# Performance work log

Hardware: AMD Instinct MI355X
Metric: run time of the kernel (lower is better)

Reference implementation:

```python
import jax, jax.numpy as jnp
import numpy as np

N = 8192        # num_nodes
H = 128         # h_dim
E = 131072      # num edges (avg degree 16)
NREL = 90       # num relations
NB = 8          # num_bases (block-diagonal decomposition)
SI = H // NB    # block size 16


def setup_inputs() -> dict:
    key = jax.random.key(0)
    ks = jax.random.split(key, 24)
    sc = 0.01
    n = lambda k, shape, s=sc: jax.random.normal(k, shape, dtype=jnp.float32) * s
    return {
        'node_ids': jnp.arange(N, dtype=jnp.int32),
        'src': jax.random.randint(ks[0], (E,), 0, N, dtype=jnp.int32),
        'dst': jax.random.randint(ks[1], (E,), 0, N, dtype=jnp.int32),
        'etypes': jax.random.randint(ks[2], (E,), 0, NREL, dtype=jnp.int32),
        'norm': jax.random.uniform(ks[3], (E, 1), dtype=jnp.float32),
        'eps': jax.random.normal(ks[4], (N, H), dtype=jnp.float32),
        # input embedding layer
        'embedding': n(ks[5], (N, H)),
        # RelGraphConv layer 0 ('bdd'): per-relation block-diag weights, self-loop, bias
        'W0': n(ks[6], (NREL, NB, SI, SI)),
        'loop0': n(ks[7], (H, H)),
        'b0': jnp.zeros((H,), jnp.float32),
        # RelGraphConv layer 1
        'W1': n(ks[8], (NREL, NB, SI, SI)),
        'loop1': n(ks[9], (H, H)),
        'b1': jnp.zeros((H,), jnp.float32),
        # z_layer: Linear(H, 2H)  (weights stored as (in, out))
        'Wz': n(ks[10], (H, 2 * H)),
        'bz': jnp.zeros((2 * H,), jnp.float32),
        # inter_layer (UpdateLayer): Linear(H, H) + h_bias
        'Wi': n(ks[11], (H, H)),
        'bi': jnp.zeros((H,), jnp.float32),
        'hbi': jnp.zeros((H,), jnp.float32),
        # output_layer (second UpdateLayer)
        'Wo': n(ks[12], (H, H)),
        'bo': jnp.zeros((H,), jnp.float32),
        'hbo': jnp.zeros((H,), jnp.float32),
    }


def _rgcn_bdd(h, W, loop_w, bias, src, dst, etypes, norm, act):
    # gather src features, split into NB blocks of size SI
    x = h[src].reshape(-1, NB, SI)                       # [E, NB, SI]
    Wg = W[etypes]                                       # [E, NB, SI, SI] per-edge relation block weights
    msg = jnp.einsum('ebi,ebio->ebo', x, Wg).reshape(-1, H) * norm  # [E, H]
    agg = jax.ops.segment_sum(msg, dst, num_segments=N)  # scatter-add to dst
    out = agg + bias + h @ loop_w                        # self-loop + bias
    return act(out) if act is not None else out


def reference(node_ids, src, dst, etypes, norm, eps, embedding,
              W0, loop0, b0, W1, loop1, b1,
              Wz, bz, Wi, bi, hbi, Wo, bo, hbo):
    # input layer: embedding lookup; saved as input_embed
    x0 = embedding[node_ids]                             # [N, H]
    h = _rgcn_bdd(x0, W0, loop0, b0, src, dst, etypes, norm, jax.nn.relu)
    h = _rgcn_bdd(h, W1, loop1, b1, src, dst, etypes, norm, None)
    # VAE head: z ~ N(mean, exp(log_std))
    zml = h @ Wz + bz                                    # [N, 2H]
    z_mean, z_log_std = jnp.split(zml, 2, axis=-1)
    z = z_mean + jnp.exp(z_log_std) * eps                # reparameterized sample
    # decode 1: outer-product reconstruction + fused update
    R = z @ z.T                                          # [N, N]
    h = R @ (z @ Wi + bi) + R @ x0 + hbi
    # decode 2
    R2 = h @ h.T                                         # [N, N]
    out = R2 @ (h @ Wo + bo) + R2 @ x0 + hbo
    return out
```

## Files before the change

### kernel.cpp

```cpp
#include <hip/hip_runtime.h>
#include <hip/hip_bf16.h>
#include <math.h>

#define Hdim 128
#define NBq 8
#define SIq 16

typedef __attribute__((ext_vector_type(8))) short short8x;
typedef __attribute__((ext_vector_type(4))) float f32x4;
typedef __attribute__((ext_vector_type(4))) unsigned short ushort4x;
typedef __attribute__((ext_vector_type(2))) _Float16 half2x;

__device__ inline unsigned short f2b(float f) {
  unsigned int u = __float_as_uint(f);
  return (unsigned short)((u + 0x7fffu + ((u >> 16) & 1u)) >> 16);
}
__device__ inline unsigned int pack2(float lo, float hi) {
  return (unsigned int)f2b(lo) | ((unsigned int)f2b(hi) << 16);
}
__device__ inline unsigned short f2h(float f) {
  _Float16 h = (_Float16)f;
  unsigned short u;
  __builtin_memcpy(&u, &h, 2);
  return u;
}
__device__ inline half2x u2h(unsigned int u) {
  union { unsigned int u; half2x h; } v;
  v.u = u;
  return v.h;
}

__global__ __launch_bounds__(256) void k_pre(
    const float* __restrict__ emb, const int* __restrict__ ids, float* __restrict__ x0,
    unsigned short* __restrict__ x0h,
    const float* __restrict__ W0, unsigned short* __restrict__ Wt0,
    const float* __restrict__ W1, unsigned short* __restrict__ Wt1, int w0elems,
    const float* __restrict__ l0, const float* __restrict__ l1,
    const float* __restrict__ Wi, const float* __restrict__ Wo, const float* __restrict__ Wz,
    unsigned short* __restrict__ l0t, unsigned short* __restrict__ l1t,
    unsigned short* __restrict__ Wit, unsigned short* __restrict__ Wot,
    unsigned short* __restrict__ Wzt,
    const int* __restrict__ dst, int* __restrict__ cnt, int E,
    int b1, int b2, int b3) {
  int bx = blockIdx.x, t = threadIdx.x;
  if (bx < b1) {
    int idx = bx * 256 + t;
    int n = idx >> 5, c4 = idx & 31;
    int s = ids[n];
    float4 v = ((const float4*)emb)[(size_t)s * 32 + c4];
    ((float4*)x0)[(size_t)n * 32 + c4] = v;
    ushort4x h;
    h.x = f2h(v.x); h.y = f2h(v.y); h.z = f2h(v.z); h.w = f2h(v.w);
    ((ushort4x*)x0h)[(size_t)n * 32 + c4] = h;
  } else if (bx < b2) {
    int idx = (bx - b1) * 256 + t;
    const float* W = (idx < w0elems) ? W0 : W1;
    unsigned short* Wt = (idx < w0elems) ? Wt0 : Wt1;
    int local = (idx < w0elems) ? idx : idx - w0elems;
    int rb = local >> 8, io = local & 255;
    int i = io >> 4, o = io & 15;
    Wt[(size_t)rb * 256 + o * 16 + i] = f2h(W[(size_t)rb * 256 + i * 16 + o]);
  } else if (bx < b3) {
    int idx = (bx - b2) * 256 + t;
    if (idx < 65536) {
      int w = idx >> 14, local = idx & 16383;
      const float* in = (w == 0) ? l0 : (w == 1) ? l1 : (w == 2) ? Wi : Wo;
      unsigned short* out = (w == 0) ? l0t : (w == 1) ? l1t : (w == 2) ? Wit : Wot;
      int n = local >> 7, k = local & 127;
      out[local] = f2b(in[k * 128 + n]);
    } else {
      int local = idx - 65536;
      int n = local >> 7, k = local & 127;
      Wzt[local] = f2b(Wz[k * 256 + n]);
    }
  } else {
    int e = (bx - b3) * 256 + t;
    if (e < E) atomicAdd(&cnt[dst[e]], 1);
  }
}

__global__ __launch_bounds__(1024) void k_scan(const int* __restrict__ cnt,
                                               int* __restrict__ off,
                                               int* __restrict__ cur, int N, int E) {
  __shared__ int part[1024];
  int t = threadIdx.x;
  int ipt = N / 1024;
  int base = t * ipt;
  int loc[8];
  int s = 0;
  for (int i = 0; i < ipt; ++i) { loc[i] = s; s += cnt[base + i]; }
  part[t] = s;
  __syncthreads();
  for (int d = 1; d < 1024; d <<= 1) {
    int v = part[t];
    int add = (t >= d) ? part[t - d] : 0;
    __syncthreads();
    part[t] = v + add;
    __syncthreads();
  }
  int pre = (t == 0) ? 0 : part[t - 1];
  for (int i = 0; i < ipt; ++i) {
    int o = pre + loc[i];
    off[base + i] = o;
    cur[base + i] = o;
  }
  if (t == 0) off[N] = E;
}

__global__ void k_scatter(const int* __restrict__ src, const int* __restrict__ dst,
                          const int* __restrict__ et, const float* __restrict__ norm,
                          int* __restrict__ cur, int* __restrict__ psrc,
                          int* __restrict__ pet, float* __restrict__ pnorm, int E) {
  int e = blockIdx.x * blockDim.x + threadIdx.x;
  if (e >= E) return;
  int p = atomicAdd(&cur[dst[e]], 1);
  psrc[p] = src[e];
  pet[p]  = et[e];
  pnorm[p] = norm[e];
}

__global__ __launch_bounds__(128) void k_edge(
    const unsigned short* __restrict__ xh, const unsigned short* __restrict__ Wt,
    const int* __restrict__ off, const int* __restrict__ psrc,
    const int* __restrict__ pet, const float* __restrict__ pnorm,
    float* __restrict__ agg) {
  int n = blockIdx.x;
  int f = threadIdx.x;
  int b = f >> 4, o = f & 15;
  int j0 = off[n], j1 = off[n + 1];
  float acc = 0.f;
#pragma unroll 2
  for (int j = j0; j < j1; ++j) {
    int s = psrc[j];
    int r = pet[j];
    float nv = pnorm[j];
    const uint4* xp = (const uint4*)(xh + (size_t)s * Hdim + b * SIq);
    const uint4* wp = (const uint4*)(Wt + ((size_t)r * NBq + b) * 256 + o * SIq);
    uint4 xa = xp[0], xc = xp[1];
    uint4 wa = wp[0], wc = wp[1];
#if __has_builtin(__builtin_amdgcn_fdot2)
    float d0 = 0.f, d1 = 0.f;
    d0 = __builtin_amdgcn_fdot2(u2h(xa.x), u2h(wa.x), d0, false);
    d1 = __builtin_amdgcn_fdot2(u2h(xa.y), u2h(wa.y), d1, false);
    d0 = __builtin_amdgcn_fdot2(u2h(xa.z), u2h(wa.z), d0, false);
    d1 = __builtin_amdgcn_fdot2(u2h(xa.w), u2h(wa.w), d1, false);
    d0 = __builtin_amdgcn_fdot2(u2h(xc.x), u2h(wc.x), d0, false);
    d1 = __builtin_amdgcn_fdot2(u2h(xc.y), u2h(wc.y), d1, false);
    d0 = __builtin_amdgcn_fdot2(u2h(xc.z), u2h(wc.z), d0, false);
    d1 = __builtin_amdgcn_fdot2(u2h(xc.w), u2h(wc.w), d1, false);
    acc = fmaf(d0 + d1, nv, acc);
#else
    float d = 0.f;
    unsigned int xu[8] = {xa.x, xa.y, xa.z, xa.w, xc.x, xc.y, xc.z, xc.w};
    unsigned int wu[8] = {wa.x, wa.y, wa.z, wa.w, wc.x, wc.y, wc.z, wc.w};
#pragma unroll
    for (int k = 0; k < 8; ++k) {
      half2x xv = u2h(xu[k]), wv = u2h(wu[k]);
      d += (float)xv.x * (float)wv.x + (float)xv.y * (float)wv.y;
    }
    acc = fmaf(d, nv, acc);
#endif
  }
  agg[(size_t)n * Hdim + f] = acc;
}

__global__ __launch_bounds__(256) void k_bgemm(
    const float* __restrict__ A, const unsigned short* __restrict__ Bt,
    const float* __restrict__ Gsrc, float* __restrict__ C,
    const float* __restrict__ addm, const float* __restrict__ bias,
    int M, int Nc, int relu, float* __restrict__ gzero,
    unsigned short* __restrict__ Ch) {
  __shared__ unsigned short Al[32][136];
  __shared__ unsigned short Bl[64][136];
  int t = threadIdx.x;
  int bm = blockIdx.x * 32, bn = blockIdx.y * 64;
  if (gzero && blockIdx.x == 0 && blockIdx.y == 0) {
#pragma unroll
    for (int i = 0; i < 16; ++i)
      ((float4*)gzero)[t + 256 * i] = make_float4(0.f, 0.f, 0.f, 0.f);
  }
  {
    int r = t >> 3, c0 = (t & 7) << 4;
    const float4* ap = (const float4*)(A + (size_t)(bm + r) * Hdim + c0);
    float4 a0 = ap[0], a1 = ap[1], a2 = ap[2], a3 = ap[3];
    uint4 p0 = { pack2(a0.x, a0.y), pack2(a0.z, a0.w), pack2(a1.x, a1.y), pack2(a1.z, a1.w) };
    uint4 p1 = { pack2(a2.x, a2.y), pack2(a2.z, a2.w), pack2(a3.x, a3.y), pack2(a3.z, a3.w) };
    *(uint4*)&Al[r][c0]     = p0;
    *(uint4*)&Al[r][c0 + 8] = p1;
  }
  if (Bt) {
    int n = t >> 2, k0 = (t & 3) << 5;
    const uint4* bp = (const uint4*)(Bt + (size_t)(bn + n) * Hdim + k0);
    uint4 b0 = bp[0], b1 = bp[1], b2 = bp[2], b3 = bp[3];
    *(uint4*)&Bl[n][k0]      = b0;
    *(uint4*)&Bl[n][k0 + 8]  = b1;
    *(uint4*)&Bl[n][k0 + 16] = b2;
    *(uint4*)&Bl[n][k0 + 24] = b3;
  } else {
    int n = t & 63, kb = (t >> 6) << 5;
    for (int i = 0; i < 32; ++i) {
      int k = kb + i;
      Bl[n][k] = f2b(Gsrc[(size_t)k * 128 + bn + n]);
    }
  }
  __syncthreads();
  int wv = t >> 6, ln = t & 63;
  int mt = wv & 1;
  int nt0 = (wv >> 1) << 1;
  int lm = ln & 15, lk = ln >> 4;
  f32x4 acc0 = {0.f, 0.f, 0.f, 0.f}, acc1 = {0.f, 0.f, 0.f, 0.f};
#pragma unroll
  for (int ks = 0; ks < 4; ++ks) {
    short8x af = *(const short8x*)&Al[mt * 16 + lm][ks * 32 + lk * 8];
    short8x bf0 = *(const short8x*)&Bl[nt0 * 16 + lm][ks * 32 + lk * 8];
    short8x bf1 = *(const short8x*)&Bl[(nt0 + 1) * 16 + lm][ks * 32 + lk * 8];
    acc0 = __builtin_amdgcn_mfma_f32_16x16x32_bf16(af, bf0, acc0, 0, 0, 0);
    acc1 = __builtin_amdgcn_mfma_f32_16x16x32_bf16(af, bf1, acc1, 0, 0, 0);
  }
  int gcol0 = bn + nt0 * 16 + lm;
  int gcol1 = gcol0 + 16;
  float b0v = bias ? bias[gcol0] : 0.f;
  float b1v = bias ? bias[gcol1] : 0.f;
#pragma unroll
  for (int reg = 0; reg < 4; ++reg) {
    int grow = bm + mt * 16 + lk * 4 + reg;
    size_t o0 = (size_t)grow * Nc + gcol0;
    size_t o1 = (size_t)grow * Nc + gcol1;
    float v0 = acc0[reg] + b0v;
    float v1 = acc1[reg] + b1v;
    if (addm) { v0 += addm[o0]; v1 += addm[o1]; }
    if (relu) { v0 = fmaxf(v0, 0.f); v1 = fmaxf(v1, 0.f); }
    C[o0] = v0;
    C[o1] = v1;
    if (Ch) { Ch[o0] = f2h(v0); Ch[o1] = f2h(v1); }
  }
}

__global__ __launch_bounds__(256) void k_bgemm_z(
    const float* __restrict__ A, const unsigned short* __restrict__ Wzt,
    const float* __restrict__ bz, const float* __restrict__ eps,
    float* __restrict__ Z, int M) {
  __shared__ unsigned short Al[32][136];
  __shared__ unsigned short Bm[64][136];
  __shared__ unsigned short Bl[64][136];
  int t = threadIdx.x;
  int bm = blockIdx.x * 32, bn = blockIdx.y * 64;
  {
    int r = t >> 3, c0 = (t & 7) << 4;
    const float4* ap = (const float4*)(A + (size_t)(bm + r) * Hdim + c0);
    float4 a0 = ap[0], a1 = ap[1], a2 = ap[2], a3 = ap[3];
    uint4 p0 = { pack2(a0.x, a0.y), pack2(a0.z, a0.w), pack2(a1.x, a1.y), pack2(a1.z, a1.w) };
    uint4 p1 = { pack2(a2.x, a2.y), pack2(a2.z, a2.w), pack2(a3.x, a3.y), pack2(a3.z, a3.w) };
    *(uint4*)&Al[r][c0]     = p0;
    *(uint4*)&Al[r][c0 + 8] = p1;
  }
  {
    int n = t >> 2, k0 = (t & 3) << 5;
    const uint4* mp = (const uint4*)(Wzt + (size_t)(bn + n) * Hdim + k0);
    const uint4* lp = (const uint4*)(Wzt + (size_t)(bn + 128 + n) * Hdim + k0);
    uint4 m0 = mp[0], m1 = mp[1], m2 = mp[2], m3 = mp[3];
    uint4 l0 = lp[0], l1 = lp[1], l2 = lp[2], l3 = lp[3];
    *(uint4*)&Bm[n][k0]      = m0; *(uint4*)&Bm[n][k0 + 8]  = m1;
    *(uint4*)&Bm[n][k0 + 16] = m2; *(uint4*)&Bm[n][k0 + 24] = m3;
    *(uint4*)&Bl[n][k0]      = l0; *(uint4*)&Bl[n][k0 + 8]  = l1;
    *(uint4*)&Bl[n][k0 + 16] = l2; *(uint4*)&Bl[n][k0 + 24] = l3;
  }
  __syncthreads();
  int wv = t >> 6, ln = t & 63;
  int mt = wv & 1;
  int nt0 = (wv >> 1) << 1;
  int lm = ln & 15, lk = ln >> 4;
  f32x4 am0 = {0,0,0,0}, am1 = {0,0,0,0}, al0 = {0,0,0,0}, al1 = {0,0,0,0};
#pragma unroll
  for (int ks = 0; ks < 4; ++ks) {
    short8x af = *(const short8x*)&Al[mt * 16 + lm][ks * 32 + lk * 8];
    short8x bm0 = *(const short8x*)&Bm[nt0 * 16 + lm][ks * 32 + lk * 8];
    short8x bm1 = *(const short8x*)&Bm[(nt0 + 1) * 16 + lm][ks * 32 + lk * 8];
    short8x bl0 = *(const short8x*)&Bl[nt0 * 16 + lm][ks * 32 + lk * 8];
    short8x bl1 = *(const short8x*)&Bl[(nt0 + 1) * 16 + lm][ks * 32 + lk * 8];
    am0 = __builtin_amdgcn_mfma_f32_16x16x32_bf16(af, bm0, am0, 0, 0, 0);
    am1 = __builtin_amdgcn_mfma_f32_16x16x32_bf16(af, bm1, am1, 0, 0, 0);
    al0 = __builtin_amdgcn_mfma_f32_16x16x32_bf16(af, bl0, al0, 0, 0, 0);
    al1 = __builtin_amdgcn_mfma_f32_16x16x32_bf16(af, bl1, al1, 0, 0, 0);
  }
  int gcol0 = bn + nt0 * 16 + lm;
  int gcol1 = gcol0 + 16;
  float bm0v = bz[gcol0], bm1v = bz[gcol1];
  float bl0v = bz[128 + gcol0], bl1v = bz[128 + gcol1];
#pragma unroll
  for (int reg = 0; reg < 4; ++reg) {
    int grow = bm + mt * 16 + lk * 4 + reg;
    size_t o0 = (size_t)grow * Hdim + gcol0;
    size_t o1 = (size_t)grow * Hdim + gcol1;
    Z[o0] = am0[reg] + bm0v + expf(al0[reg] + bl0v) * eps[o0];
    Z[o1] = am1[reg] + bm1v + expf(al1[reg] + bl1v) * eps[o1];
  }
}

__global__ __launch_bounds__(256) void k_xty(const float* __restrict__ X,
                                             const float* __restrict__ Y,
                                             float* __restrict__ G, int N) {
  __shared__ float xs[8][64];
  __shared__ float ys[8][64];
  int t  = threadIdx.x;
  int tx = t & 15, ty = t >> 4;
  int qr = blockIdx.y >> 1, qc = blockIdx.y & 1;
  int KC = N / gridDim.x;
  int k0 = blockIdx.x * KC;
  int m  = t >> 7, li = t & 127;
  int lr = li >> 4, lc = (li & 15) << 2;
  const float* S = m ? Y : X;
  int coff = (m ? qc : qr) * 64;
  float acc[4][4] = {};
  for (int kb = 0; kb < KC; kb += 8) {
    float4 v = *(const float4*)(S + (size_t)(k0 + kb + lr) * Hdim + coff + lc);
    __syncthreads();
    if (m) *(float4*)&ys[lr][lc] = v; else *(float4*)&xs[lr][lc] = v;
    __syncthreads();
#pragma unroll
    for (int kk = 0; kk < 8; ++kk) {
      float4 xv = *(const float4*)&xs[kk][ty << 2];
      float4 yv = *(const float4*)&ys[kk][tx << 2];
      acc[0][0] += xv.x * yv.x; acc[0][1] += xv.x * yv.y; acc[0][2] += xv.x * yv.z; acc[0][3] += xv.x * yv.w;
      acc[1][0] += xv.y * yv.x; acc[1][1] += xv.y * yv.y; acc[1][2] += xv.y * yv.z; acc[1][3] += xv.y * yv.w;
      acc[2][0] += xv.z * yv.x; acc[2][1] += xv.z * yv.y; acc[2][2] += xv.z * yv.z; acc[2][3] += xv.z * yv.w;
      acc[3][0] += xv.w * yv.x; acc[3][1] += xv.w * yv.y; acc[3][2] += xv.w * yv.z; acc[3][3] += xv.w * yv.w;
    }
  }
  int grow = qr * 64 + (ty << 2);
  int gcol = qc * 64 + (tx << 2);
#pragma unroll
  for (int r = 0; r < 4; ++r)
#pragma unroll
    for (int c = 0; c < 4; ++c)
      atomicAdd(&G[(size_t)(grow + r) * Hdim + gcol + c], acc[r][c]);
}

extern "C" void kernel_launch(void* const* d_in, const int* in_sizes, int n_in,
                              void* d_out, int out_size, void* d_ws, size_t ws_size,
                              hipStream_t stream) {
  const int*   node_ids = (const int*)d_in[0];
  const int*   src      = (const int*)d_in[1];
  const int*   dst      = (const int*)d_in[2];
  const int*   et       = (const int*)d_in[3];
  const float* norm     = (const float*)d_in[4];
  const float* eps      = (const float*)d_in[5];
  const float* emb      = (const float*)d_in[6];
  const float* W0       = (const float*)d_in[7];
  const float* loop0    = (const float*)d_in[8];
  const float* b0       = (const float*)d_in[9];
  const float* W1       = (const float*)d_in[10];
  const float* loop1    = (const float*)d_in[11];
  const float* b1       = (const float*)d_in[12];
  const float* Wz       = (const float*)d_in[13];
  const float* bz       = (const float*)d_in[14];
  const float* Wi       = (const float*)d_in[15];
  const float* bi       = (const float*)d_in[16];
  const float* hbi      = (const float*)d_in[17];
  const float* Wo       = (const float*)d_in[18];
  const float* bo       = (const float*)d_in[19];
  const float* hbo      = (const float*)d_in[20];
  float* out = (float*)d_out;

  const int N  = in_sizes[0];
  const int E  = in_sizes[1];
  const int RB = in_sizes[7] / (SIq * SIq);

  char* ws = (char*)d_ws;
  const size_t MB = 1u << 20;
  const size_t KB = 1u << 10;
  float* X0   = (float*)(ws + 0 * MB);
  float* B1p  = (float*)(ws + 4 * MB);
  float* B2p  = (float*)(ws + 8 * MB);
  float* AGG  = (float*)(ws + 12 * MB);
  float* B3p  = (float*)(ws + 16 * MB);
  float* G    = (float*)(ws + 20 * MB);
  int*   offp = (int*)(ws + 20 * MB + 256 * KB);
  int*   curp = (int*)(ws + 20 * MB + 512 * KB);
  int*   cntp = (int*)(ws + 20 * MB + 768 * KB);
  int*   psrc = (int*)(ws + 21 * MB);
  int*   pet  = (int*)(ws + 21 * MB + 512 * KB);
  float* pnrm = (float*)(ws + 22 * MB);
  unsigned short* Wt0 = (unsigned short*)(ws + 22 * MB + 512 * KB);
  unsigned short* Wt1 = (unsigned short*)(ws + 23 * MB);
  unsigned short* l0t = (unsigned short*)(ws + 24 * MB);
  unsigned short* l1t = (unsigned short*)(ws + 24 * MB + 64 * KB);
  unsigned short* Wit = (unsigned short*)(ws + 24 * MB + 128 * KB);
  unsigned short* Wot = (unsigned short*)(ws + 24 * MB + 192 * KB);
  unsigned short* Wzt = (unsigned short*)(ws + 24 * MB + 256 * KB);
  unsigned short* X0H = (unsigned short*)(ws + 25 * MB);
  unsigned short* B1H = (unsigned short*)(ws + 27 * MB);

  dim3 blk(256);

  const int w0elems = RB * 256;
  const int gB   = (N * 32) / 256;
  const int wtbB = (2 * w0elems + 255) / 256;
  const int wttB = 98304 / 256;
  const int histB = (E + 255) / 256;
  const int b1s = gB, b2s = gB + wtbB, b3s = gB + wtbB + wttB;
  hipMemsetAsync(cntp, 0, (size_t)N * sizeof(int), stream);
  k_pre<<<dim3(b3s + histB), blk, 0, stream>>>(
      emb, node_ids, X0, X0H, W0, Wt0, W1, Wt1, w0elems,
      loop0, loop1, Wi, Wo, Wz, l0t, l1t, Wit, Wot, Wzt,
      dst, cntp, E, b1s, b2s, b3s);
  k_scan<<<dim3(1), dim3(1024), 0, stream>>>(cntp, offp, curp, N, E);
  k_scatter<<<dim3((E + 255) / 256), blk, 0, stream>>>(src, dst, et, norm, curp,
                                                       psrc, pet, pnrm, E);

  k_edge<<<dim3(N), dim3(128), 0, stream>>>(X0H, Wt0, offp, psrc, pet, pnrm, AGG);
  k_bgemm<<<dim3(N / 32, 2), blk, 0, stream>>>(X0, l0t, nullptr, B1p, AGG, b0, N, Hdim, 1, nullptr, B1H);
  k_edge<<<dim3(N), dim3(128), 0, stream>>>(B1H, Wt1, offp, psrc, pet, pnrm, AGG);
  k_bgemm<<<dim3(N / 32, 2), blk, 0, stream>>>(B1p, l1t, nullptr, B2p, AGG, b1, N, Hdim, 0, nullptr, nullptr);
  k_bgemm_z<<<dim3(N / 32, 2), blk, 0, stream>>>(B2p, Wzt, bz, eps, B1p, N);
  k_bgemm<<<dim3(N / 32, 2), blk, 0, stream>>>(B1p, Wit, nullptr, B3p, X0, bi, N, Hdim, 0, G, nullptr);
  k_xty<<<dim3(32, 4), blk, 0, stream>>>(B1p, B3p, G, N);
  k_bgemm<<<dim3(N / 32, 2), blk, 0, stream>>>(B1p, nullptr, G, B2p, nullptr, hbi, N, Hdim, 0, nullptr, nullptr);
  k_bgemm<<<dim3(N / 32, 2), blk, 0, stream>>>(B2p, Wot, nullptr, B3p, X0, bo, N, Hdim, 0, G, nullptr);
  k_xty<<<dim3(32, 4), blk, 0, stream>>>(B2p, B3p, G, N);
  k_bgemm<<<dim3(N / 32, 2), blk, 0, stream>>>(B2p, nullptr, G, out, nullptr, hbo, N, Hdim, 0, nullptr, nullptr);
}
```

Baseline: 297.2 us.

## Collapse both decode stages into small Gram matrices computed in one fixup kernel

The two sequential decode stages are rewritten algebraically. Only Z^T Z, Z^T X0 and column sums are accumulated over the nodes, and a single-block kernel then combines them into a 128x128 matrix and a bias vector, so the final output becomes one N x 128 GEMM from Z. This removes the intermediate N x 128 passes for h and the second Gram reduction. Edge metadata is also packed into one int4 record so each edge needs a single load. The cost is a serial single-block kernel of several 128-cubed GEMMs and more bf16 rounding through chained products, which may affect accuracy.

New measurement: 317.0 us. 1.07x slower.

```diff
diff --git a/kernel.cpp b/kernel.cpp
--- a/kernel.cpp
+++ b/kernel.cpp
@@ -5,6 +5,7 @@
 #define Hdim 128
 #define NBq 8
 #define SIq 16
+#define LDP 136
 
 typedef __attribute__((ext_vector_type(8))) short short8x;
 typedef __attribute__((ext_vector_type(4))) float f32x4;
@@ -109,20 +110,16 @@
 
 __global__ void k_scatter(const int* __restrict__ src, const int* __restrict__ dst,
                           const int* __restrict__ et, const float* __restrict__ norm,
-                          int* __restrict__ cur, int* __restrict__ psrc,
-                          int* __restrict__ pet, float* __restrict__ pnorm, int E) {
+                          int* __restrict__ cur, int4* __restrict__ pedge, int E) {
   int e = blockIdx.x * blockDim.x + threadIdx.x;
   if (e >= E) return;
   int p = atomicAdd(&cur[dst[e]], 1);
-  psrc[p] = src[e];
-  pet[p]  = et[e];
-  pnorm[p] = norm[e];
+  pedge[p] = make_int4(src[e], et[e], __float_as_int(norm[e]), 0);
 }
 
 __global__ __launch_bounds__(128) void k_edge(
     const unsigned short* __restrict__ xh, const unsigned short* __restrict__ Wt,
-    const int* __restrict__ off, const int* __restrict__ psrc,
-    const int* __restrict__ pet, const float* __restrict__ pnorm,
+    const int* __restrict__ off, const int4* __restrict__ pedge,
     float* __restrict__ agg) {
   int n = blockIdx.x;
   int f = threadIdx.x;
@@ -131,9 +128,10 @@
   float acc = 0.f;
 #pragma unroll 2
   for (int j = j0; j < j1; ++j) {
-    int s = psrc[j];
-    int r = pet[j];
-    float nv = pnorm[j];
+    int4 meta = pedge[j];
+    int s = meta.x;
+    int r = meta.y;
+    float nv = __int_as_float(meta.z);
     const uint4* xp = (const uint4*)(xh + (size_t)s * Hdim + b * SIq);
     const uint4* wp = (const uint4*)(Wt + ((size_t)r * NBq + b) * 256 + o * SIq);
     uint4 xa = xp[0], xc = xp[1];
@@ -166,19 +164,13 @@
 
 __global__ __launch_bounds__(256) void k_bgemm(
     const float* __restrict__ A, const unsigned short* __restrict__ Bt,
-    const float* __restrict__ Gsrc, float* __restrict__ C,
+    float* __restrict__ C,
     const float* __restrict__ addm, const float* __restrict__ bias,
-    int M, int Nc, int relu, float* __restrict__ gzero,
-    unsigned short* __restrict__ Ch) {
+    int M, int Nc, int relu, unsigned short* __restrict__ Ch) {
   __shared__ unsigned short Al[32][136];
   __shared__ unsigned short Bl[64][136];
   int t = threadIdx.x;
   int bm = blockIdx.x * 32, bn = blockIdx.y * 64;
-  if (gzero && blockIdx.x == 0 && blockIdx.y == 0) {
-#pragma unroll
-    for (int i = 0; i < 16; ++i)
-      ((float4*)gzero)[t + 256 * i] = make_float4(0.f, 0.f, 0.f, 0.f);
-  }
   {
     int r = t >> 3, c0 = (t & 7) << 4;
     const float4* ap = (const float4*)(A + (size_t)(bm + r) * Hdim + c0);
@@ -188,7 +180,7 @@
     *(uint4*)&Al[r][c0]     = p0;
     *(uint4*)&Al[r][c0 + 8] = p1;
   }
-  if (Bt) {
+  {
     int n = t >> 2, k0 = (t & 3) << 5;
     const uint4* bp = (const uint4*)(Bt + (size_t)(bn + n) * Hdim + k0);
     uint4 b0 = bp[0], b1 = bp[1], b2 = bp[2], b3 = bp[3];
@@ -196,12 +188,6 @@
     *(uint4*)&Bl[n][k0 + 8]  = b1;
     *(uint4*)&Bl[n][k0 + 16] = b2;
     *(uint4*)&Bl[n][k0 + 24] = b3;
-  } else {
-    int n = t & 63, kb = (t >> 6) << 5;
-    for (int i = 0; i < 32; ++i) {
-      int k = kb + i;
-      Bl[n][k] = f2b(Gsrc[(size_t)k * 128 + bn + n]);
-    }
   }
   __syncthreads();
   int wv = t >> 6, ln = t & 63;
@@ -239,12 +225,19 @@
 __global__ __launch_bounds__(256) void k_bgemm_z(
     const float* __restrict__ A, const unsigned short* __restrict__ Wzt,
     const float* __restrict__ bz, const float* __restrict__ eps,
-    float* __restrict__ Z, int M) {
+    float* __restrict__ Z, int M, float* __restrict__ gz) {
   __shared__ unsigned short Al[32][136];
   __shared__ unsigned short Bm[64][136];
   __shared__ unsigned short Bl[64][136];
   int t = threadIdx.x;
   int bm = blockIdx.x * 32, bn = blockIdx.y * 64;
+  if (gz && blockIdx.x == 0 && blockIdx.y == 0) {
+#pragma unroll
+    for (int i = 0; i < 9; ++i) {
+      int idx = t + 256 * i;
+      if (idx < 2064) ((float4*)gz)[idx] = make_float4(0.f, 0.f, 0.f, 0.f);
+    }
+  }
   {
     int r = t >> 3, c0 = (t & 7) << 4;
     const float4* ap = (const float4*)(A + (size_t)(bm + r) * Hdim + c0);
@@ -297,23 +290,30 @@
   }
 }
 
-__global__ __launch_bounds__(256) void k_xty(const float* __restrict__ X,
-                                             const float* __restrict__ Y,
-                                             float* __restrict__ G, int N) {
+__global__ __launch_bounds__(256) void k_xty2(const float* __restrict__ Z,
+                                              const float* __restrict__ X0,
+                                              float* __restrict__ SP,
+                                              float* __restrict__ s1,
+                                              float* __restrict__ cx0, int N) {
   __shared__ float xs[8][64];
   __shared__ float ys[8][64];
   int t  = threadIdx.x;
   int tx = t & 15, ty = t >> 4;
-  int qr = blockIdx.y >> 1, qc = blockIdx.y & 1;
+  int qr = blockIdx.y >> 2;
+  int qc = blockIdx.y & 3;
   int KC = N / gridDim.x;
   int k0 = blockIdx.x * KC;
   int m  = t >> 7, li = t & 127;
   int lr = li >> 4, lc = (li & 15) << 2;
-  const float* S = m ? Y : X;
-  int coff = (m ? qc : qr) * 64;
+  const float* S = m ? ((qc < 2) ? Z : X0) : Z;
+  int coff = m ? ((qc & 1) * 64) : (qr * 64);
+  bool do_s1 = (!m) && (qc == 0);
+  bool do_cx = m && (qr == 0) && (qc >= 2);
+  float csum[4] = {0.f, 0.f, 0.f, 0.f};
   float acc[4][4] = {};
   for (int kb = 0; kb < KC; kb += 8) {
     float4 v = *(const float4*)(S + (size_t)(k0 + kb + lr) * Hdim + coff + lc);
+    if (do_s1 || do_cx) { csum[0] += v.x; csum[1] += v.y; csum[2] += v.z; csum[3] += v.w; }
     __syncthreads();
     if (m) *(float4*)&ys[lr][lc] = v; else *(float4*)&xs[lr][lc] = v;
     __syncthreads();
@@ -333,7 +333,151 @@
   for (int r = 0; r < 4; ++r)
 #pragma unroll
     for (int c = 0; c < 4; ++c)
-      atomicAdd(&G[(size_t)(grow + r) * Hdim + gcol + c], acc[r][c]);
+      atomicAdd(&SP[(size_t)(grow + r) * 256 + gcol + c], acc[r][c]);
+  if (do_s1) {
+#pragma unroll
+    for (int i = 0; i < 4; ++i) atomicAdd(&s1[coff + lc + i], csum[i]);
+  }
+  if (do_cx) {
+#pragma unroll
+    for (int i = 0; i < 4; ++i) atomicAdd(&cx0[coff + lc + i], csum[i]);
+  }
+}
+
+__device__ inline void stage_f32(unsigned short* dst, const float* __restrict__ src,
+                                 int ldF, int t) {
+#pragma unroll
+  for (int it = 0; it < 8; ++it) {
+    int id = it * 256 + t; int row = id >> 4, ch = id & 15;
+    const float4* gp = (const float4*)(src + (size_t)row * ldF) + ch * 2;
+    float4 u = gp[0], v = gp[1];
+    uint4 pk = { pack2(u.x, u.y), pack2(u.z, u.w), pack2(v.x, v.y), pack2(v.z, v.w) };
+    *(uint4*)&dst[row * LDP + ch * 8] = pk;
+  }
+}
+__device__ inline void stage_b16(unsigned short* dst, const unsigned short* __restrict__ src,
+                                 int t) {
+#pragma unroll
+  for (int it = 0; it < 8; ++it) {
+    int id = it * 256 + t; int row = id >> 4, ch = id & 15;
+    *(uint4*)&dst[row * LDP + ch * 8] = ((const uint4*)(src + (size_t)row * 128))[ch];
+  }
+}
+__device__ inline void stage_f32T(unsigned short* dst, const float* __restrict__ src,
+                                  int ldF, int t) {
+#pragma unroll
+  for (int it = 0; it < 8; ++it) {
+    int id = it * 256 + t; int n = id >> 4, ig = id & 15;
+    unsigned short tmp[8];
+#pragma unroll
+    for (int u = 0; u < 8; ++u) tmp[u] = f2b(src[(size_t)(ig * 8 + u) * ldF + n]);
+    uint4 pk;
+    __builtin_memcpy(&pk, tmp, 16);
+    *(uint4*)&dst[n * LDP + ig * 8] = pk;
+  }
+}
+__device__ inline void mm128(const unsigned short* A, const unsigned short* B,
+                             f32x4 (&Cc)[2][8], int wv, int lm, int lk) {
+#pragma unroll
+  for (int ks = 0; ks < 4; ++ks) {
+    short8x af0 = *(const short8x*)&A[(wv * 32 + lm) * LDP + ks * 32 + lk * 8];
+    short8x af1 = *(const short8x*)&A[(wv * 32 + 16 + lm) * LDP + ks * 32 + lk * 8];
+#pragma unroll
+    for (int ni = 0; ni < 8; ++ni) {
+      short8x bf = *(const short8x*)&B[(ni * 16 + lm) * LDP + ks * 32 + lk * 8];
+      Cc[0][ni] = __builtin_amdgcn_mfma_f32_16x16x32_bf16(af0, bf, Cc[0][ni], 0, 0, 0);
+      Cc[1][ni] = __builtin_amdgcn_mfma_f32_16x16x32_bf16(af1, bf, Cc[1][ni], 0, 0, 0);
+    }
+  }
+}
+#define ZEROC {                                           \
+  _Pragma("unroll") for (int mi = 0; mi < 2; ++mi)        \
+  _Pragma("unroll") for (int ni = 0; ni < 8; ++ni)        \
+    C[mi][ni] = (f32x4){0.f, 0.f, 0.f, 0.f}; }
+#define CLOOP(body) {                                     \
+  _Pragma("unroll") for (int mi = 0; mi < 2; ++mi)        \
+  _Pragma("unroll") for (int ni = 0; ni < 8; ++ni)        \
+  _Pragma("unroll") for (int rg = 0; rg < 4; ++rg) {      \
+    int grow = wv * 32 + mi * 16 + lk * 4 + rg;           \
+    int gcol = ni * 16 + lm;                              \
+    float v = C[mi][ni][rg];                              \
+    body;                                                 \
+  } }
+
+__global__ __launch_bounds__(256) void k_fix(
+    const float* __restrict__ SP, const float* __restrict__ s1g,
+    const float* __restrict__ cx0g,
+    const unsigned short* __restrict__ Wit, const unsigned short* __restrict__ Wot,
+    const float* __restrict__ bi, const float* __restrict__ hbi,
+    const float* __restrict__ bo, const float* __restrict__ hbo,
+    float* __restrict__ G1g, float* __restrict__ G1tg, float* __restrict__ A2g,
+    float* __restrict__ P2g, float* __restrict__ S2g, float* __restrict__ G2tg,
+    unsigned short* __restrict__ G12t, float* __restrict__ bvec, float Nf) {
+  __shared__ unsigned short Asl[128 * LDP];
+  __shared__ unsigned short Bsl[128 * LDP];
+  __shared__ float s1l[128], tl[128], s2l[128], cxl[128], bil[128], bol[128], hl[128];
+  int t = threadIdx.x;
+  int wv = t >> 6, ln = t & 63, lm = ln & 15, lk = ln >> 4;
+  if (t < 128) {
+    s1l[t] = s1g[t]; cxl[t] = cx0g[t]; bil[t] = bi[t]; bol[t] = bo[t]; hl[t] = hbi[t];
+  }
+  f32x4 C[2][8];
+  stage_f32(Asl, SP, 256, t);
+  stage_b16(Bsl, Wit, t);
+  __syncthreads();
+  ZEROC; mm128(Asl, Bsl, C, wv, lm, lk);
+  CLOOP({
+    v += s1l[grow] * bil[gcol] + SP[(size_t)grow * 256 + 128 + gcol];
+    G1g[grow * 128 + gcol] = v;
+    G1tg[gcol * 128 + grow] = v;
+  });
+  __syncthreads();
+  if (t < 128) {
+    float a2 = 0.f;
+    for (int i = 0; i < 128; ++i) a2 += G1tg[t * 128 + i] * s1l[i];
+    tl[t] = a2; s2l[t] = a2 + Nf * hl[t];
+  }
+  __syncthreads();
+  stage_f32(Asl, G1tg, 128, t);
+  stage_f32(Bsl, SP, 256, t);
+  __syncthreads();
+  ZEROC; mm128(Asl, Bsl, C, wv, lm, lk);
+  CLOOP({ A2g[grow * 128 + gcol] = v; });
+  __syncthreads();
+  stage_f32T(Bsl, SP + 128, 256, t);
+  __syncthreads();
+  ZEROC; mm128(Asl, Bsl, C, wv, lm, lk);
+  CLOOP({ v += hl[grow] * cxl[gcol]; P2g[grow * 128 + gcol] = v; });
+  __syncthreads();
+  stage_f32(Asl, A2g, 128, t);
+  stage_f32(Bsl, G1tg, 128, t);
+  __syncthreads();
+  ZEROC; mm128(Asl, Bsl, C, wv, lm, lk);
+  CLOOP({
+    v += tl[grow] * hl[gcol] + hl[grow] * tl[gcol] + Nf * hl[grow] * hl[gcol];
+    S2g[grow * 128 + gcol] = v;
+  });
+  __syncthreads();
+  stage_f32(Asl, S2g, 128, t);
+  stage_b16(Bsl, Wot, t);
+  __syncthreads();
+  ZEROC; mm128(Asl, Bsl, C, wv, lm, lk);
+  CLOOP({
+    v += s2l[grow] * bol[gcol] + P2g[grow * 128 + gcol];
+    G2tg[gcol * 128 + grow] = v;
+  });
+  __syncthreads();
+  stage_f32(Asl, G1g, 128, t);
+  stage_f32(Bsl, G2tg, 128, t);
+  __syncthreads();
+  ZEROC; mm128(Asl, Bsl, C, wv, lm, lk);
+  CLOOP({ G12t[gcol * 128 + grow] = f2b(v); });
+  __syncthreads();
+  if (t < 128) {
+    float a2 = 0.f;
+    for (int i = 0; i < 128; ++i) a2 += hl[i] * G2tg[t * 128 + i];
+    bvec[t] = a2 + hbo[t];
+  }
 }
 
 extern "C" void kernel_launch(void* const* d_in, const int* in_sizes, int n_in,
@@ -373,16 +517,23 @@
   float* B1p  = (float*)(ws + 4 * MB);
   float* B2p  = (float*)(ws + 8 * MB);
   float* AGG  = (float*)(ws + 12 * MB);
-  float* B3p  = (float*)(ws + 16 * MB);
-  float* G    = (float*)(ws + 20 * MB);
-  int*   offp = (int*)(ws + 20 * MB + 256 * KB);
-  int*   curp = (int*)(ws + 20 * MB + 512 * KB);
-  int*   cntp = (int*)(ws + 20 * MB + 768 * KB);
-  int*   psrc = (int*)(ws + 21 * MB);
-  int*   pet  = (int*)(ws + 21 * MB + 512 * KB);
-  float* pnrm = (float*)(ws + 22 * MB);
-  unsigned short* Wt0 = (unsigned short*)(ws + 22 * MB + 512 * KB);
-  unsigned short* Wt1 = (unsigned short*)(ws + 23 * MB);
+  float* SPb  = (float*)(ws + 16 * MB);
+  float* s1p  = SPb + 32768;
+  float* cx0p = SPb + 32896;
+  float* G1g  = (float*)(ws + 16 * MB + 192 * KB);
+  float* G1tg = (float*)(ws + 16 * MB + 256 * KB);
+  float* A2g  = (float*)(ws + 16 * MB + 320 * KB);
+  float* P2g  = (float*)(ws + 16 * MB + 384 * KB);
+  float* S2g  = (float*)(ws + 16 * MB + 448 * KB);
+  float* G2tg = (float*)(ws + 16 * MB + 512 * KB);
+  unsigned short* G12t = (unsigned short*)(ws + 16 * MB + 576 * KB);
+  float* bvec = (float*)(ws + 16 * MB + 640 * KB);
+  int*   offp = (int*)(ws + 20 * MB);
+  int*   curp = (int*)(ws + 20 * MB + 256 * KB);
+  int*   cntp = (int*)(ws + 20 * MB + 512 * KB);
+  int4*  pedge = (int4*)(ws + 21 * MB);
+  unsigned short* Wt0 = (unsigned short*)(ws + 23 * MB);
+  unsigned short* Wt1 = (unsigned short*)(ws + 23 * MB + 512 * KB);
   unsigned short* l0t = (unsigned short*)(ws + 24 * MB);
   unsigned short* l1t = (unsigned short*)(ws + 24 * MB + 64 * KB);
   unsigned short* Wit = (unsigned short*)(ws + 24 * MB + 128 * KB);
@@ -405,18 +556,16 @@
       loop0, loop1, Wi, Wo, Wz, l0t, l1t, Wit, Wot, Wzt,
       dst, cntp, E, b1s, b2s, b3s);
   k_scan<<<dim3(1), dim3(1024), 0, stream>>>(cntp, offp, curp, N, E);
-  k_scatter<<<dim3((E + 255) / 256), blk, 0, stream>>>(src, dst, et, norm, curp,
-                                                       psrc, pet, pnrm, E);
-
-  k_edge<<<dim3(N), dim3(128), 0, stream>>>(X0H, Wt0, offp, psrc, pet, pnrm, AGG);
-  k_bgemm<<<dim3(N / 32, 2), blk, 0, stream>>>(X0, l0t, nullptr, B1p, AGG, b0, N, Hdim, 1, nullptr, B1H);
-  k_edge<<<dim3(N), dim3(128), 0, stream>>>(B1H, Wt1, offp, psrc, pet, pnrm, AGG);
-  k_bgemm<<<dim3(N / 32, 2), blk, 0, stream>>>(B1p, l1t, nullptr, B2p, AGG, b1, N, Hdim, 0, nullptr, nullptr);
-  k_bgemm_z<<<dim3(N / 32, 2), blk, 0, stream>>>(B2p, Wzt, bz, eps, B1p, N);
-  k_bgemm<<<dim3(N / 32, 2), blk, 0, stream>>>(B1p, Wit, nullptr, B3p, X0, bi, N, Hdim, 0, G, nullptr);
-  k_xty<<<dim3(32, 4), blk, 0, stream>>>(B1p, B3p, G, N);
-  k_bgemm<<<dim3(N / 32, 2), blk, 0, stream>>>(B1p, nullptr, G, B2p, nullptr, hbi, N, Hdim, 0, nullptr, nullptr);
-  k_bgemm<<<dim3(N / 32, 2), blk, 0, stream>>>(B2p, Wot, nullptr, B3p, X0, bo, N, Hdim, 0, G, nullptr);
-  k_xty<<<dim3(32, 4), blk, 0, stream>>>(B2p, B3p, G, N);
-  k_bgemm<<<dim3(N / 32, 2), blk, 0, stream>>>(B2p, nullptr, G, out, nullptr, hbo, N, Hdim, 0, nullptr, nullptr);
-}
+  k_scatter<<<dim3((E + 255) / 256), blk, 0, stream>>>(src, dst, et, norm, curp, pedge, E);
+
+  k_edge<<<dim3(N), dim3(128), 0, stream>>>(X0H, Wt0, offp, pedge, AGG);
+  k_bgemm<<<dim3(N / 32, 2), blk, 0, stream>>>(X0, l0t, B1p, AGG, b0, N, Hdim, 1, B1H);
+  k_edge<<<dim3(N), dim3(128), 0, stream>>>(B1H, Wt1, offp, pedge, AGG);
+  k_bgemm<<<dim3(N / 32, 2), blk, 0, stream>>>(B1p, l1t, B2p, AGG, b1, N, Hdim, 0, nullptr);
+  k_bgemm_z<<<dim3(N / 32, 2), blk, 0, stream>>>(B2p, Wzt, bz, eps, B1p, N, SPb);
+  k_xty2<<<dim3(32, 8), blk, 0, stream>>>(B1p, X0, SPb, s1p, cx0p, N);
+  k_fix<<<dim3(1), blk, 0, stream>>>(SPb, s1p, cx0p, Wit, Wot, bi, hbi, bo, hbo,
+                                     G1g, G1tg, A2g, P2g, S2g, G2tg, G12t, bvec,
+                                     (float)N);
+  k_bgemm<<<dim3(N / 32, 2), blk, 0, stream>>>(B1p, G12t, out, nullptr, bvec, N, Hdim, 0, nullptr);
+}
```
